# Kernel optimization log

Measured on AMD Instinct MI355X. Metric: run time of the kernel, lower is better.

The kernel has to match this reference:

```python
import jax, jax.numpy as jnp
import numpy as np

N = 262144      # number of points
K = 16          # KNN neighbors -> fixed degree CSR
E = N * K
CLASS_DIM = 40


def setup_inputs() -> dict:
    key = jax.random.key(0)
    ks = jax.random.split(key, 12)
    x = jax.random.normal(ks[0], (N, 3), dtype=jnp.float32)
    indptr = (jnp.arange(N + 1, dtype=jnp.int32) * K)
    indices = jax.random.randint(ks[1], (E,), 0, N, dtype=jnp.int32)

    def xavier(k, fan_out, fan_in):
        bound = np.sqrt(6.0 / (fan_in + fan_out)).astype(np.float32)
        return jax.random.uniform(k, (fan_out, fan_in), dtype=jnp.float32,
                                  minval=-bound, maxval=bound)

    return {
        "x": x, "indptr": indptr, "indices": indices,
        "w1": xavier(ks[2], 64, 3),
        "w2": xavier(ks[3], 64, 64),
        "w3": xavier(ks[4], 64, 64),
        "w4": xavier(ks[5], 128, 64),
        "w5": xavier(ks[6], 1024, 192),
        "wf1": xavier(ks[7], 512, 1024),
        "wf2": xavier(ks[8], 256, 512),
        "wf3": xavier(ks[9], CLASS_DIM, 256),
    }


def reference(x, indptr, indices, w1, w2, w3, w4, w5, wf1, wf2, wf3):
    # mlp1, mlp2 (bias-free Linear + ReLU)
    h = jax.nn.relu(x @ w1.T)          # [N, 64]
    h = jax.nn.relu(h @ w2.T)          # [N, 64]

    # GraphMaxPooling: CSR neighbor max (segment-max over gathered rows)
    n = h.shape[0]
    e = indices.shape[0]
    deg = indptr[1:] - indptr[:-1]                                   # [N]
    seg = jnp.repeat(jnp.arange(n, dtype=jnp.int32), deg,
                     total_repeat_length=e)                          # [E]
    x_gm = jax.ops.segment_max(h[indices], seg, num_segments=n,
                               indices_are_sorted=True)              # [N, 64]

    # mlp3, mlp4
    h3 = jax.nn.relu(h @ w3.T)         # [N, 64]
    h4 = jax.nn.relu(h3 @ w4.T)        # [N, 128]

    # concat neighbor-pooled features with point features, mlp5
    hc = jnp.concatenate([x_gm, h4], axis=1)   # [N, 192]
    h5 = jax.nn.relu(hc @ w5.T)                # [N, 1024]

    # global max pool over points -> [1, 1024]
    g = jnp.max(h5, axis=0, keepdims=True)

    # classifier head (dropout in eval mode = identity)
    f = jax.nn.relu(g @ wf1.T)
    f = jax.nn.relu(f @ wf2.T)
    return f @ wf3.T                            # [1, class_dim]
```

## Files before the change

kernel.cpp:

```cpp
#include <hip/hip_runtime.h>
#include <hip/hip_bf16.h>
#include <stdint.h>

typedef unsigned short u16;
typedef __bf16 bf16x8 __attribute__((ext_vector_type(8)));
typedef float  f32x4  __attribute__((ext_vector_type(4)));
typedef u16    u16x8  __attribute__((ext_vector_type(8)));

__device__ __forceinline__ float bf2f(u16 u) {
    return __uint_as_float(((unsigned)u) << 16);
}
__device__ __forceinline__ u16 f2bf(float f) {
    unsigned u = __float_as_uint(f);
    u += 0x7fffu + ((u >> 16) & 1u);
    return (u16)(u >> 16);
}
__device__ __forceinline__ u16x8 maxu16(u16x8 a, u16x8 b) {
    u16x8 r;
    #pragma unroll
    for (int e = 0; e < 8; ++e) r[e] = a[e] > b[e] ? a[e] : b[e];
    return r;
}

#define MFMA16(a, b, c) __builtin_amdgcn_mfma_f32_16x16x32_bf16(a, b, c, 0, 0, 0)

__device__ u16   h2g_buf[262144 * 64];
__device__ u16   w3b[64 * 64];
__device__ u16   w4b[128 * 64];
__device__ u16   w5t[64 * 6 * 64 * 8];
__device__ float g_buf[1024];
__device__ float f1_buf[512];
__device__ float f2_buf[256];

__global__ void k0_zero() { g_buf[threadIdx.x] = 0.f; }

__global__ void kcvt(const float* __restrict__ w3f, const float* __restrict__ w4f,
                     const float* __restrict__ w5f)
{
    int i = blockIdx.x * 256 + threadIdx.x;
    if (i < 4096)        w3b[i]        = f2bf(w3f[i]);
    else if (i < 12288)  w4b[i - 4096] = f2bf(w4f[i - 4096]);
    else {
        int o    = i - 12288;
        int e    = o & 7;
        int lane = (o >> 3) & 63;
        int sg   = o >> 9;
        int s    = sg % 6, c16 = sg / 6;
        int q    = lane >> 4, l15 = lane & 15;
        w5t[o] = f2bf(w5f[(c16 * 16 + l15) * 192 + s * 32 + q * 8 + e]);
    }
}

__global__ __launch_bounds__(256) void k1_mlp(
    const float* __restrict__ xf, const float* __restrict__ w1f,
    const float* __restrict__ w2f)
{
    __shared__ __align__(16) u16 sw1[64 * 4];
    __shared__ __align__(16) u16 sx [64 * 4];
    __shared__ __align__(16) u16 sw2[64 * 72];
    __shared__ __align__(16) u16 shA[64 * 72];
    __shared__ __align__(16) u16 sh2[64 * 72];

    const int tid = threadIdx.x;
    const int p0  = blockIdx.x * 64;

    for (int i = tid; i < 64 * 64; i += 256)
        sw2[(i >> 6) * 72 + (i & 63)] = f2bf(w2f[i]);
    if (tid < 192) {
        sw1[(tid / 3) * 4 + tid % 3] = f2bf(w1f[tid]);
        sx [(tid / 3) * 4 + tid % 3] = f2bf(xf[p0 * 3 + tid]);
    }
    __syncthreads();

    {
        int m = tid & 63, ng = tid >> 6;
        float x0 = bf2f(sx[m * 4]), x1 = bf2f(sx[m * 4 + 1]), x2 = bf2f(sx[m * 4 + 2]);
        #pragma unroll
        for (int j = 0; j < 16; ++j) {
            int n = ng * 16 + j;
            float s = x0 * bf2f(sw1[n * 4]) + x1 * bf2f(sw1[n * 4 + 1]) + x2 * bf2f(sw1[n * 4 + 2]);
            shA[m * 72 + n] = f2bf(fmaxf(s, 0.f));
        }
    }
    __syncthreads();

    const int lane = tid & 63, w = tid >> 6, q = lane >> 4, l15 = lane & 15;
    const int mrow = 16 * w;

    f32x4 acc2[4];
    #pragma unroll
    for (int nt = 0; nt < 4; ++nt) acc2[nt] = (f32x4){0.f, 0.f, 0.f, 0.f};
    #pragma unroll
    for (int s = 0; s < 2; ++s) {
        bf16x8 a = *(const bf16x8*)&shA[(mrow + l15) * 72 + s * 32 + q * 8];
        #pragma unroll
        for (int nt = 0; nt < 4; ++nt) {
            bf16x8 b = *(const bf16x8*)&sw2[(nt * 16 + l15) * 72 + s * 32 + q * 8];
            acc2[nt] = MFMA16(a, b, acc2[nt]);
        }
    }
    #pragma unroll
    for (int nt = 0; nt < 4; ++nt)
        #pragma unroll
        for (int r = 0; r < 4; ++r) {
            int m = mrow + q * 4 + r;
            sh2[m * 72 + nt * 16 + l15] = f2bf(fmaxf(acc2[nt][r], 0.f));
        }
    __syncthreads();

    {
        int row = tid >> 2, c = (tid & 3) * 16;
        *(u16x8*)&h2g_buf[(size_t)p0 * 64 + tid * 16]     = *(const u16x8*)&sh2[row * 72 + c];
        *(u16x8*)&h2g_buf[(size_t)p0 * 64 + tid * 16 + 8] = *(const u16x8*)&sh2[row * 72 + c + 8];
    }
}

__global__ __launch_bounds__(512) void k3_fused(const int* __restrict__ idx,
                                                int* __restrict__ gout)
{
    __shared__ __align__(16) u16 lds[36864];
    u16* p0  = lds;
    u16* p1  = lds + 8192;
    u16* p2  = lds + 16384;
    u16* sw3 = lds + 24576;
    u16* sw4 = lds + 28672;

    const int tid  = threadIdx.x;
    const int lane = tid & 63, w = tid >> 6, q = lane >> 4, l15 = lane & 15;
    const size_t R0 = (size_t)blockIdx.x * 128;

    #pragma unroll
    for (int c = 0; c < 2; ++c) {
        int task = c * 512 + tid;
        int r = task >> 3, jc = task & 7;
        const int* ip = &idx[(R0 + r) * 16];
        u16x8 v[16];
        #pragma unroll
        for (int k = 0; k < 16; ++k)
            v[k] = *(const u16x8*)&h2g_buf[(size_t)ip[k] * 64 + jc * 8];
        #pragma unroll
        for (int o = 8; o; o >>= 1)
            #pragma unroll
            for (int k = 0; k < o; ++k) v[k] = maxu16(v[k], v[k + o]);
        *(u16x8*)&p0[r * 64 + ((jc ^ r) & 7) * 8] = v[0];
    }

    {
        int r = tid >> 3, js = tid & 7;
        *(u16x8*)&sw3[r * 64 + ((js ^ r) & 7) * 8] = *(const u16x8*)&w3b[r * 64 + js * 8];
        #pragma unroll
        for (int c = 0; c < 2; ++c) {
            int i = c * 512 + tid, r4 = i >> 3, j4 = i & 7;
            *(u16x8*)&sw4[r4 * 64 + ((j4 ^ r4) & 7) * 8] = *(const u16x8*)&w4b[r4 * 64 + j4 * 8];
        }
        #pragma unroll
        for (int c = 0; c < 2; ++c) {
            int i = c * 512 + tid, ra = i >> 3, ja = i & 7;
            *(u16x8*)&p1[ra * 64 + ((ja ^ ra) & 7) * 8] =
                *(const u16x8*)&h2g_buf[(R0 + ra) * 64 + ja * 8];
        }
    }
    __syncthreads();

    {
        f32x4 a3[4];
        #pragma unroll
        for (int nt = 0; nt < 4; ++nt) a3[nt] = (f32x4){0.f, 0.f, 0.f, 0.f};
        #pragma unroll
        for (int ss = 0; ss < 2; ++ss) {
            int js = ss * 4 + q, r = w * 16 + l15;
            bf16x8 a = *(const bf16x8*)&p1[r * 64 + ((js ^ r) & 7) * 8];
            #pragma unroll
            for (int nt = 0; nt < 4; ++nt) {
                int rw = nt * 16 + l15;
                bf16x8 b = *(const bf16x8*)&sw3[rw * 64 + ((js ^ rw) & 7) * 8];
                a3[nt] = MFMA16(a, b, a3[nt]);
            }
        }
        #pragma unroll
        for (int nt = 0; nt < 4; ++nt)
            #pragma unroll
            for (int r = 0; r < 4; ++r) {
                int m = w * 16 + q * 4 + r;
                int n = nt * 16 + l15;
                p2[m * 64 + (((n >> 3) ^ m) & 7) * 8 + (n & 7)] =
                    f2bf(fmaxf(a3[nt][r], 0.f));
            }
    }

    {
        f32x4 a4[8];
        #pragma unroll
        for (int nt = 0; nt < 8; ++nt) a4[nt] = (f32x4){0.f, 0.f, 0.f, 0.f};
        #pragma unroll
        for (int ss = 0; ss < 2; ++ss) {
            int js = ss * 4 + q, r = w * 16 + l15;
            bf16x8 a = *(const bf16x8*)&p2[r * 64 + ((js ^ r) & 7) * 8];
            #pragma unroll
            for (int nt = 0; nt < 8; ++nt) {
                int rw = nt * 16 + l15;
                bf16x8 b = *(const bf16x8*)&sw4[rw * 64 + ((js ^ rw) & 7) * 8];
                a4[nt] = MFMA16(a, b, a4[nt]);
            }
        }
        #pragma unroll
        for (int nt = 0; nt < 8; ++nt)
            #pragma unroll
            for (int r = 0; r < 4; ++r) {
                int m  = w * 16 + q * 4 + r;
                int n4 = nt * 16 + l15;
                int j  = (n4 >> 3) & 7;
                u16* dp = (nt < 4) ? p1 : p2;
                dp[m * 64 + ((j ^ m) & 7) * 8 + (n4 & 7)] = f2bf(fmaxf(a4[nt][r], 0.f));
            }
    }
    __syncthreads();

    #pragma unroll 1
    for (int cg = 0; cg < 4; ++cg) {
        f32x4 acc[8][2];
        #pragma unroll
        for (int mt = 0; mt < 8; ++mt)
            #pragma unroll
            for (int nt = 0; nt < 2; ++nt) acc[mt][nt] = (f32x4){0.f, 0.f, 0.f, 0.f};
        #pragma unroll
        for (int s = 0; s < 6; ++s) {
            const u16* pa = (s < 2) ? p0 : ((s < 4) ? p1 : p2);
            int j = (s & 1) * 4 + q;
            bf16x8 b[2];
            #pragma unroll
            for (int nt = 0; nt < 2; ++nt)
                b[nt] = *(const bf16x8*)&w5t[(size_t)(((cg * 16 + w * 2 + nt) * 6 + s)) * 512 + lane * 8];
            bf16x8 a[8];
            #pragma unroll
            for (int mt = 0; mt < 8; ++mt) {
                int r = mt * 16 + l15;
                a[mt] = *(const bf16x8*)&pa[r * 64 + ((j ^ r) & 7) * 8];
            }
            #pragma unroll
            for (int mt = 0; mt < 8; ++mt)
                #pragma unroll
                for (int nt = 0; nt < 2; ++nt)
                    acc[mt][nt] = MFMA16(a[mt], b[nt], acc[mt][nt]);
        }

        #pragma unroll
        for (int nt = 0; nt < 2; ++nt) {
            float mx = 0.f;
            #pragma unroll
            for (int mt = 0; mt < 8; ++mt)
                #pragma unroll
                for (int e = 0; e < 4; ++e) mx = fmaxf(mx, acc[mt][nt][e]);
            mx = fmaxf(mx, __shfl_xor(mx, 16, 64));
            mx = fmaxf(mx, __shfl_xor(mx, 32, 64));
            if (q == 0)
                atomicMax(&gout[cg * 256 + w * 32 + nt * 16 + l15], __float_as_int(mx));
        }
    }
}

__global__ void k4_f1(const float* __restrict__ wf1)
{
    int r = blockIdx.x, l = threadIdx.x;
    float s = 0.f;
    #pragma unroll
    for (int i = 0; i < 16; ++i) s += wf1[r * 1024 + i * 64 + l] * g_buf[i * 64 + l];
    #pragma unroll
    for (int o = 32; o; o >>= 1) s += __shfl_down(s, o, 64);
    if (!l) f1_buf[r] = fmaxf(s, 0.f);
}
__global__ void k4_f2(const float* __restrict__ wf2)
{
    int r = blockIdx.x, l = threadIdx.x;
    float s = 0.f;
    #pragma unroll
    for (int i = 0; i < 8; ++i) s += wf2[r * 512 + i * 64 + l] * f1_buf[i * 64 + l];
    #pragma unroll
    for (int o = 32; o; o >>= 1) s += __shfl_down(s, o, 64);
    if (!l) f2_buf[r] = fmaxf(s, 0.f);
}
__global__ void k4_out(const float* __restrict__ wf3, float* __restrict__ out)
{
    int r = blockIdx.x, l = threadIdx.x;
    float s = 0.f;
    #pragma unroll
    for (int i = 0; i < 4; ++i) s += wf3[r * 256 + i * 64 + l] * f2_buf[i * 64 + l];
    #pragma unroll
    for (int o = 32; o; o >>= 1) s += __shfl_down(s, o, 64);
    if (!l) out[r] = s;
}

extern "C" void kernel_launch(void* const* d_in, const int* in_sizes, int n_in,
                              void* d_out, int out_size, void* d_ws, size_t ws_size,
                              hipStream_t stream)
{
    (void)in_sizes; (void)n_in; (void)out_size; (void)d_ws; (void)ws_size;
    const float* x   = (const float*)d_in[0];
    const int*   idx = (const int*)d_in[2];
    const float* w1  = (const float*)d_in[3];
    const float* w2  = (const float*)d_in[4];
    const float* w3  = (const float*)d_in[5];
    const float* w4  = (const float*)d_in[6];
    const float* w5  = (const float*)d_in[7];
    const float* wf1 = (const float*)d_in[8];
    const float* wf2 = (const float*)d_in[9];
    const float* wf3 = (const float*)d_in[10];

    float* gptr;
    hipGetSymbolAddress((void**)&gptr, HIP_SYMBOL(g_buf));

    k0_zero <<<1, 1024, 0, stream>>>();
    kcvt    <<<816, 256, 0, stream>>>(w3, w4, w5);
    k1_mlp  <<<262144 / 64, 256, 0, stream>>>(x, w1, w2);
    k3_fused<<<2048, 512, 0, stream>>>(idx, (int*)gptr);
    k4_f1   <<<512, 64, 0, stream>>>(wf1);
    k4_f2   <<<256, 64, 0, stream>>>(wf2);
    k4_out  <<<40, 64, 0, stream>>>(wf3, (float*)d_out);
}
```

Baseline: 474.3 us.

## Split neighbor max-pool gather into separate kernel before fused MLP kernel

Moves the CSR neighbor gather and max out of the large fused MLP kernel into its own lightweight kernel that writes pooled features to a new global buffer, which the fused kernel then loads like the point features. The intent is to let the latency-bound random gather run at high occupancy without the fused kernel's LDS and register footprint, and to simplify the fused kernel's prologue. It also adds an opaque zero offset to the LDS A-operand reads, to stop the compiler from hoisting or rescheduling those loads across the column-group loop. In exchange the pooled features make an extra round trip through global memory, and there is one more kernel launch.

```diff
diff --git a/kernel.cpp b/kernel.cpp
--- a/kernel.cpp
+++ b/kernel.cpp
@@ -25,6 +25,7 @@
 #define MFMA16(a, b, c) __builtin_amdgcn_mfma_f32_16x16x32_bf16(a, b, c, 0, 0, 0)
 
 __device__ u16   h2g_buf[262144 * 64];
+__device__ u16   gm_buf [262144 * 64];
 __device__ u16   w3b[64 * 64];
 __device__ u16   w4b[128 * 64];
 __device__ u16   w5t[64 * 6 * 64 * 8];
@@ -115,8 +116,25 @@
     }
 }
 
-__global__ __launch_bounds__(512) void k3_fused(const int* __restrict__ idx,
-                                                int* __restrict__ gout)
+__global__ __launch_bounds__(256) void k2_pool(const int* __restrict__ idx)
+{
+    const size_t gt = (size_t)blockIdx.x * 256 + threadIdx.x;
+    const size_t p  = gt >> 3;
+    const int    c  = (threadIdx.x & 7) * 8;
+
+    u16x8 v[16];
+    #pragma unroll
+    for (int k = 0; k < 16; ++k) {
+        int j = idx[p * 16 + k];
+        v[k] = *(const u16x8*)&h2g_buf[(size_t)j * 64 + c];
+    }
+    u16x8 m = v[0];
+    #pragma unroll
+    for (int k = 1; k < 16; ++k) m = maxu16(m, v[k]);
+    *(u16x8*)&gm_buf[p * 64 + c] = m;
+}
+
+__global__ __launch_bounds__(512) void k3_fused(int* __restrict__ gout)
 {
     __shared__ __align__(16) u16 lds[36864];
     u16* p0  = lds;
@@ -129,22 +147,6 @@
     const int lane = tid & 63, w = tid >> 6, q = lane >> 4, l15 = lane & 15;
     const size_t R0 = (size_t)blockIdx.x * 128;
 
-    #pragma unroll
-    for (int c = 0; c < 2; ++c) {
-        int task = c * 512 + tid;
-        int r = task >> 3, jc = task & 7;
-        const int* ip = &idx[(R0 + r) * 16];
-        u16x8 v[16];
-        #pragma unroll
-        for (int k = 0; k < 16; ++k)
-            v[k] = *(const u16x8*)&h2g_buf[(size_t)ip[k] * 64 + jc * 8];
-        #pragma unroll
-        for (int o = 8; o; o >>= 1)
-            #pragma unroll
-            for (int k = 0; k < o; ++k) v[k] = maxu16(v[k], v[k + o]);
-        *(u16x8*)&p0[r * 64 + ((jc ^ r) & 7) * 8] = v[0];
-    }
-
     {
         int r = tid >> 3, js = tid & 7;
         *(u16x8*)&sw3[r * 64 + ((js ^ r) & 7) * 8] = *(const u16x8*)&w3b[r * 64 + js * 8];
@@ -156,6 +158,8 @@
         #pragma unroll
         for (int c = 0; c < 2; ++c) {
             int i = c * 512 + tid, ra = i >> 3, ja = i & 7;
+            *(u16x8*)&p0[ra * 64 + ((ja ^ ra) & 7) * 8] =
+                *(const u16x8*)&gm_buf[(R0 + ra) * 64 + ja * 8];
             *(u16x8*)&p1[ra * 64 + ((ja ^ ra) & 7) * 8] =
                 *(const u16x8*)&h2g_buf[(R0 + ra) * 64 + ja * 8];
         }
@@ -216,8 +220,10 @@
     }
     __syncthreads();
 
+    int zoff = 0;
     #pragma unroll 1
     for (int cg = 0; cg < 4; ++cg) {
+        asm volatile("" : "+v"(zoff));
         f32x4 acc[8][2];
         #pragma unroll
         for (int mt = 0; mt < 8; ++mt)
@@ -235,7 +241,7 @@
             #pragma unroll
             for (int mt = 0; mt < 8; ++mt) {
                 int r = mt * 16 + l15;
-                a[mt] = *(const bf16x8*)&pa[r * 64 + ((j ^ r) & 7) * 8];
+                a[mt] = *(const bf16x8*)&pa[r * 64 + ((j ^ r) & 7) * 8 + zoff];
             }
             #pragma unroll
             for (int mt = 0; mt < 8; ++mt)
@@ -312,7 +318,8 @@
     k0_zero <<<1, 1024, 0, stream>>>();
     kcvt    <<<816, 256, 0, stream>>>(w3, w4, w5);
     k1_mlp  <<<262144 / 64, 256, 0, stream>>>(x, w1, w2);
-    k3_fused<<<2048, 512, 0, stream>>>(idx, (int*)gptr);
+    k2_pool <<<262144 * 8 / 256, 256, 0, stream>>>(idx);
+    k3_fused<<<2048, 512, 0, stream>>>((int*)gptr);
     k4_f1   <<<512, 64, 0, stream>>>(wf1);
     k4_f2   <<<256, 64, 0, stream>>>(wf2);
     k4_out  <<<40, 64, 0, stream>>>(wf3, (float*)d_out);
```

Result: faster. 388.0 us (-18.2%).
